# Kernel optimization log

Measured on AMD Instinct MI355X. Metric: run time of the kernel, lower is better.

## Reference

```python
import math
import jax, jax.numpy as jnp
import numpy as np

T_STEPS = 1000
NU = 1e-3
EPS = 1.0
MU = 1.0
DT = 0.01


def _ddx(f):
    # central difference d/dx on last dim, periodic
    return (jnp.roll(f, -1, -1) - jnp.roll(f, 1, -1)) * 0.5


def _ddy(f):
    return (jnp.roll(f, -1, -2) - jnp.roll(f, 1, -2)) * 0.5


def _laplacian(f):
    return (jnp.roll(f, 1, -1) + jnp.roll(f, -1, -1)
            + jnp.roll(f, 1, -2) + jnp.roll(f, -1, -2) - 4.0 * f)


def _cosine_betas(T, s=0.008):
    steps = jnp.arange(T + 1, dtype=jnp.float32)
    ac = jnp.cos((steps / T + s) / (1.0 + s) * (math.pi * 0.5)) ** 2
    ac = ac / ac[0]
    betas = 1.0 - ac[1:] / ac[:-1]
    return jnp.clip(betas, 0.0, 0.999)


def _wavenumbers(H, W):
    ky = jnp.fft.fftfreq(H, 1.0 / H).astype(jnp.float32).reshape(H, 1)
    kx = jnp.fft.rfftfreq(W, 1.0 / W).astype(jnp.float32).reshape(1, W // 2 + 1)
    return ky, kx


def _poisson_fft(rhs):
    # solve lap(phi) = rhs on periodic domain via rfft2
    H, W = rhs.shape[-2:]
    rhs_f = jnp.fft.rfft2(rhs)
    ky, kx = _wavenumbers(H, W)
    k2 = jnp.maximum(kx ** 2 + ky ** 2, 1e-10).at[0, 0].set(1.0)
    phi_f = rhs_f / (-4.0 * math.pi ** 2 * k2)
    phi_f = phi_f.at[:, 0, 0].set(0.0)
    return jnp.fft.irfft2(phi_f, s=(H, W))


def _project_div_free(Jx, Jy):
    H, W = Jx.shape[-2:]
    Jxf = jnp.fft.rfft2(Jx)
    Jyf = jnp.fft.rfft2(Jy)
    ky, kx = _wavenumbers(H, W)
    k2 = jnp.maximum(kx ** 2 + ky ** 2, 1e-10)
    div_f = kx * Jxf + ky * Jyf
    Jxf = Jxf - kx * div_f / k2
    Jyf = Jyf - ky * div_f / k2
    return jnp.fft.irfft2(Jxf, s=(H, W)), jnp.fft.irfft2(Jyf, s=(H, W))


def _l2_normalize(f):
    # F.normalize over flattened spatial dims per batch element
    norm = jnp.sqrt(jnp.sum(f * f, axis=(1, 2), keepdims=True))
    return f / jnp.maximum(norm, 1e-12)


def _forward(x0, noise, f_u, f_v, jx, jy, t):
    betas = _cosine_betas(T_STEPS)
    ac = jnp.cumprod(1.0 - betas)
    s_alpha = jnp.sqrt(ac)[t].reshape(-1, 1, 1, 1)
    s_one = jnp.sqrt(1.0 - ac)[t].reshape(-1, 1, 1, 1)
    sqrt_beta = jnp.sqrt(betas)[t].reshape(-1, 1, 1)

    # q_sample: x_t = sqrt(abar_t) x0 + sqrt(1-abar_t) eps
    xt = s_alpha * x0 + s_one * noise

    # ---- Navier-Stokes explicit Euler step (channels 0..2 = u,v,p) ----
    u, v, p = xt[:, 0], xt[:, 1], xt[:, 2]
    adv_u = u * _ddx(u) + v * _ddy(u)
    adv_v = u * _ddx(v) + v * _ddy(v)
    diff_u = NU * _laplacian(u)
    diff_v = NU * _laplacian(v)
    dp_dx, dp_dy = _ddx(p), _ddy(p)
    fu, fv = f_u, f_v
    for _ in range(3):  # fixed smoothing iterations
        fu = fu + 0.1 * _laplacian(fu)
        fv = fv + 0.1 * _laplacian(fv)
    fu = _l2_normalize(fu)
    fv = _l2_normalize(fv)
    u_new = u + DT * (-adv_u + diff_u - dp_dx) + sqrt_beta * fu
    v_new = v + DT * (-adv_v + diff_v - dp_dy) + sqrt_beta * fv
    div = _ddx(u_new) + _ddy(v_new)
    p_corr = _poisson_fft(div)
    u_new = u_new - _ddx(p_corr)
    v_new = v_new - _ddy(p_corr)
    p_new = p + p_corr

    # ---- Maxwell TM Yee half-step (channels 3..5 = Ex,Ey,Bz) ----
    Ex, Ey, Bz = xt[:, 3], xt[:, 4], xt[:, 5]
    Jx = jx * sqrt_beta
    Jy = jy * sqrt_beta
    Jx, Jy = _project_div_free(Jx, Jy)
    curl_E = _ddx(Ey) - _ddy(Ex)
    Bz_new = Bz - (DT / MU) * curl_E
    Ex_new = Ex + (DT / EPS) * _ddy(Bz_new) - (DT / EPS) * Jx
    Ey_new = Ey - (DT / EPS) * _ddx(Bz_new) - (DT / EPS) * Jy

    return jnp.stack([u_new, v_new, p_new, Ex_new, Ey_new, Bz_new], axis=1)


def setup_inputs() -> dict:
    key = jax.random.key(0)
    ks = jax.random.split(key, 7)
    B, C, H, W = 16, 6, 512, 512
    return {
        "x0": jax.random.normal(ks[0], (B, C, H, W), dtype=jnp.float32),
        "noise": jax.random.normal(ks[1], (B, C, H, W), dtype=jnp.float32),
        "f_u": jax.random.normal(ks[2], (B, H, W), dtype=jnp.float32),
        "f_v": jax.random.normal(ks[3], (B, H, W), dtype=jnp.float32),
        "jx": jax.random.normal(ks[4], (B, H, W), dtype=jnp.float32),
        "jy": jax.random.normal(ks[5], (B, H, W), dtype=jnp.float32),
        "t": jax.random.randint(ks[6], (B,), 0, 1000, dtype=jnp.int32),
    }


def reference(x0, noise, f_u, f_v, jx, jy, t):
    return _forward(x0, noise, f_u, f_v, jx, jy, t)
```

## Files before the change

kernel.cpp:

```cpp
#include <hip/hip_runtime.h>
#include <math.h>

#define PI2SQ4 39.478417604357434f
#define FSTRIDE 545
#define IDX(i) ((i) + ((i) >> 4))

__device__ __forceinline__ void wave_fence() {
  asm volatile("" ::: "memory");
  __builtin_amdgcn_wave_barrier();
}

__device__ __forceinline__ float4 ld4(const float* p) {
  return *reinterpret_cast<const float4*>(p);
}
__device__ __forceinline__ void st4(float* p, float4 v) {
  *reinterpret_cast<float4*>(p) = v;
}
__device__ __forceinline__ float fc(const float4& v, int j) {
  return j == 0 ? v.x : j == 1 ? v.y : j == 2 ? v.z : v.w;
}
__device__ __forceinline__ float fc8(const float4& a, const float4& b, int j) {
  return j < 4 ? fc(a, j) : fc(b, j - 4);
}
__device__ __forceinline__ float4 xtl4(const float* x0, const float* ns, int off,
                                       float sa, float so) {
  float4 a = ld4(x0 + off), b = ld4(ns + off);
  return make_float4(sa * a.x + so * b.x, sa * a.y + so * b.y,
                     sa * a.z + so * b.z, sa * a.w + so * b.w);
}

__device__ void wave_fft512(float2* s, const float2* tw, int lane, float isign) {
  wave_fence();
#pragma unroll
  for (int k = 0; k < 8; ++k) {
    int i = lane + (k << 6);
    int r = (int)(__brev((unsigned)i) >> 23);
    if (i < r) { float2 a = s[IDX(i)]; float2 b = s[IDX(r)]; s[IDX(i)] = b; s[IDX(r)] = a; }
  }
  wave_fence();
  for (int st = 0; st < 9; ++st) {
    int half = 1 << st;
#pragma unroll
    for (int k = 0; k < 4; ++k) {
      int bf = lane + (k << 6);
      int j = bf & (half - 1);
      int i0 = ((bf >> st) << (st + 1)) + j;
      int i1 = i0 + half;
      float2 w = tw[j << (8 - st)];
      float cw = w.x, sw = w.y * isign;
      float2 a = s[IDX(i0)], b = s[IDX(i1)];
      float tr = b.x * cw - b.y * sw;
      float ti = b.x * sw + b.y * cw;
      s[IDX(i0)] = make_float2(a.x + tr, a.y + ti);
      s[IDX(i1)] = make_float2(a.x - tr, a.y - ti);
    }
    wave_fence();
  }
}

__device__ __forceinline__ void tw_init(float2* tw, int tid) {
  if (tid < 256) {
    float sw, cw;
    __sincosf((float)tid * -0.012271846303085128f, &sw, &cw);
    tw[tid] = make_float2(cw, sw);
  }
}

__global__ __launch_bounds__(1024) void k_coef(const int* __restrict__ t,
                                               float* __restrict__ coef,
                                               float* __restrict__ norms) {
  __shared__ double l[1024];
  int i = threadIdx.x;
  if (i < 32) norms[i] = 0.f;
  const double s = 0.008;
  const double HPI = 1.5707963267948966;
  double val = 0.0;
  if (i < 1000) {
    double c0 = cos(((double)i / 1000.0 + s) / (1.0 + s) * HPI);
    double c1 = cos(((double)(i + 1) / 1000.0 + s) / (1.0 + s) * HPI);
    double beta = 1.0 - (c1 * c1) / (c0 * c0);
    beta = fmin(fmax(beta, 0.0), 0.999);
    val = log1p(-beta);
  }
  l[i] = val;
  __syncthreads();
  for (int off = 1; off < 1024; off <<= 1) {
    double add = (i >= off) ? l[i - off] : 0.0;
    __syncthreads();
    l[i] += add;
    __syncthreads();
  }
  if (i < 16) {
    int tt = t[i];
    double ac = exp(l[tt]);
    double c0 = cos(((double)tt / 1000.0 + s) / (1.0 + s) * HPI);
    double c1 = cos(((double)(tt + 1) / 1000.0 + s) / (1.0 + s) * HPI);
    double beta = 1.0 - (c1 * c1) / (c0 * c0);
    beta = fmin(fmax(beta, 0.0), 0.999);
    coef[i * 4 + 0] = (float)sqrt(ac);
    coef[i * 4 + 1] = (float)sqrt(1.0 - ac);
    coef[i * 4 + 2] = (float)sqrt(beta);
  }
}

__global__ __launch_bounds__(256) void k_smooth3(const float* __restrict__ fu,
                                                 const float* __restrict__ fv,
                                                 float* __restrict__ dst,
                                                 float* __restrict__ norms) {
  __shared__ float sA[70 * 71];
  __shared__ float sB[70 * 71];
  __shared__ float part[4];
  int slab = blockIdx.x >> 6;
  int tile = blockIdx.x & 63;
  int tx0 = (tile & 7) << 6, ty0 = (tile >> 3) << 6;
  int b = slab & 15;
  const float* src = ((slab >> 4) ? fv : fu) + ((size_t)b << 18);
  int tid = threadIdx.x;

  for (int idx = tid; idx < 70 * 70; idx += 256) {
    int cy = idx / 70, cx = idx - cy * 70;
    int gx = (tx0 + cx - 3) & 511, gy = (ty0 + cy - 3) & 511;
    sA[cy * 71 + cx] = src[(gy << 9) + gx];
  }
  __syncthreads();
  for (int idx = tid; idx < 68 * 68; idx += 256) {
    int cy = idx / 68 + 1, cx = idx % 68 + 1;
    int o = cy * 71 + cx;
    float c = sA[o];
    sB[o] = c + 0.1f * (sA[o - 1] + sA[o + 1] + sA[o - 71] + sA[o + 71] - 4.f * c);
  }
  __syncthreads();
  for (int idx = tid; idx < 66 * 66; idx += 256) {
    int cy = idx / 66 + 2, cx = idx % 66 + 2;
    int o = cy * 71 + cx;
    float c = sB[o];
    sA[o] = c + 0.1f * (sB[o - 1] + sB[o + 1] + sB[o - 71] + sB[o + 71] - 4.f * c);
  }
  __syncthreads();
  float acc = 0.f;
  float* d = dst + ((size_t)slab << 18);
  for (int idx = tid; idx < 64 * 64; idx += 256) {
    int cy = (idx >> 6) + 3, cx = (idx & 63) + 3;
    int o = cy * 71 + cx;
    float c = sA[o];
    float v = c + 0.1f * (sA[o - 1] + sA[o + 1] + sA[o - 71] + sA[o + 71] - 4.f * c);
    d[((ty0 + cy - 3) << 9) + (tx0 + cx - 3)] = v;
    acc += v * v;
  }
  for (int off = 32; off; off >>= 1) acc += __shfl_down(acc, off, 64);
  if ((tid & 63) == 0) part[tid >> 6] = acc;
  __syncthreads();
  if (tid == 0) atomicAdd(&norms[slab], part[0] + part[1] + part[2] + part[3]);
}

#define XTLS(cb, i) (sa * x0[(cb) + (i)] + so * ns[(cb) + (i)])

__global__ __launch_bounds__(256) void k_star(const float* __restrict__ x0,
    const float* __restrict__ ns, const float* __restrict__ fA,
    const float* __restrict__ coef, const float* __restrict__ norms,
    float* __restrict__ us, float* __restrict__ vs) {
  int gid = blockIdx.x * 256 + threadIdx.x;
  int x4 = (gid & 127) << 2;
  int y = (gid >> 7) & 511, b = gid >> 16;
  float sa = coef[b * 4], so = coef[b * 4 + 1], sb = coef[b * 4 + 2];
  int row = y << 9;
  int rowm = ((y + 511) & 511) << 9, rowp = ((y + 1) & 511) << 9;
  int xl = (x4 + 511) & 511, xr = (x4 + 4) & 511;
  int c0 = (b * 6) << 18, c1 = (b * 6 + 1) << 18, c2 = (b * 6 + 2) << 18;

  float4 uC = xtl4(x0, ns, c0 + row + x4, sa, so);
  float4 uU = xtl4(x0, ns, c0 + rowm + x4, sa, so);
  float4 uD = xtl4(x0, ns, c0 + rowp + x4, sa, so);
  float ulw = XTLS(c0, row + xl), urx = XTLS(c0, row + xr);
  float4 vC = xtl4(x0, ns, c1 + row + x4, sa, so);
  float4 vU = xtl4(x0, ns, c1 + rowm + x4, sa, so);
  float4 vD = xtl4(x0, ns, c1 + rowp + x4, sa, so);
  float vlw = XTLS(c1, row + xl), vrx = XTLS(c1, row + xr);
  float4 pC = xtl4(x0, ns, c2 + row + x4, sa, so);
  float4 pU = xtl4(x0, ns, c2 + rowm + x4, sa, so);
  float4 pD = xtl4(x0, ns, c2 + rowp + x4, sa, so);
  float plw = XTLS(c2, row + xl), prx = XTLS(c2, row + xr);

  float rnu = 1.f / fmaxf(sqrtf(norms[b]), 1e-12f);
  float rnv = 1.f / fmaxf(sqrtf(norms[16 + b]), 1e-12f);
  int bb = b << 18;
  float4 fu4 = ld4(fA + bb + row + x4);
  float4 fv4 = ld4(fA + ((16 + b) << 18) + row + x4);

  float ru[4], rv[4];
#pragma unroll
  for (int j = 0; j < 4; ++j) {
    float u_c = fc(uC, j), v_c = fc(vC, j);
    float u_xm = j == 0 ? ulw : fc(uC, j - 1);
    float u_xp = j == 3 ? urx : fc(uC, j + 1);
    float v_xm = j == 0 ? vlw : fc(vC, j - 1);
    float v_xp = j == 3 ? vrx : fc(vC, j + 1);
    float p_xm = j == 0 ? plw : fc(pC, j - 1);
    float p_xp = j == 3 ? prx : fc(pC, j + 1);
    float u_ym = fc(uU, j), u_yp = fc(uD, j);
    float v_ym = fc(vU, j), v_yp = fc(vD, j);
    float p_ym = fc(pU, j), p_yp = fc(pD, j);
    float adv_u = u_c * 0.5f * (u_xp - u_xm) + v_c * 0.5f * (u_yp - u_ym);
    float adv_v = u_c * 0.5f * (v_xp - v_xm) + v_c * 0.5f * (v_yp - v_ym);
    float dif_u = 0.001f * (u_xm + u_xp + u_ym + u_yp - 4.f * u_c);
    float dif_v = 0.001f * (v_xm + v_xp + v_ym + v_yp - 4.f * v_c);
    float dpx = 0.5f * (p_xp - p_xm), dpy = 0.5f * (p_yp - p_ym);
    ru[j] = u_c + 0.01f * (-adv_u + dif_u - dpx) + sb * fc(fu4, j) * rnu;
    rv[j] = v_c + 0.01f * (-adv_v + dif_v - dpy) + sb * fc(fv4, j) * rnv;
  }
  st4(us + bb + row + x4, make_float4(ru[0], ru[1], ru[2], ru[3]));
  st4(vs + bb + row + x4, make_float4(rv[0], rv[1], rv[2], rv[3]));
}

__global__ __launch_bounds__(256) void k_rowfft_div(const float* __restrict__ us,
    const float* __restrict__ vs, float2* __restrict__ spec) {
  __shared__ float2 buf[4 * FSTRIDE];
  __shared__ float2 tw[256];
  int tid = threadIdx.x;
  tw_init(tw, tid);
  int wave = tid >> 6, lane = tid & 63;
  int rid = (blockIdx.x << 2) + wave;
  int pb = rid >> 9, y = rid & 511;
  int rym = ((y + 511) & 511) << 9, ryp = ((y + 1) & 511) << 9, ry = y << 9;
  const float* ul = us + ((size_t)pb << 18);
  const float* vl = vs + ((size_t)pb << 18);
  const float* uh = us + ((size_t)(pb + 8) << 18);
  const float* vh = vs + ((size_t)(pb + 8) << 18);
  float2* s = buf + wave * FSTRIDE;
  int xx0 = lane << 3;
  int xl = (xx0 + 511) & 511, xr = (xx0 + 8) & 511;
  float4 ulA = ld4(ul + ry + xx0), ulB = ld4(ul + ry + xx0 + 4);
  float ullw = ul[ry + xl], ulrx = ul[ry + xr];
  float4 vlU0 = ld4(vl + rym + xx0), vlU1 = ld4(vl + rym + xx0 + 4);
  float4 vlD0 = ld4(vl + ryp + xx0), vlD1 = ld4(vl + ryp + xx0 + 4);
  float4 uhA = ld4(uh + ry + xx0), uhB = ld4(uh + ry + xx0 + 4);
  float uhlw = uh[ry + xl], uhrx = uh[ry + xr];
  float4 vhU0 = ld4(vh + rym + xx0), vhU1 = ld4(vh + rym + xx0 + 4);
  float4 vhD0 = ld4(vh + ryp + xx0), vhD1 = ld4(vh + ryp + xx0 + 4);
  __syncthreads();
#pragma unroll
  for (int j = 0; j < 8; ++j) {
    float uxm = j == 0 ? ullw : fc8(ulA, ulB, j - 1);
    float uxp = j == 7 ? ulrx : fc8(ulA, ulB, j + 1);
    float dlo = 0.5f * (uxp - uxm) + 0.5f * (fc8(vlD0, vlD1, j) - fc8(vlU0, vlU1, j));
    float hxm = j == 0 ? uhlw : fc8(uhA, uhB, j - 1);
    float hxp = j == 7 ? uhrx : fc8(uhA, uhB, j + 1);
    float dhi = 0.5f * (hxp - hxm) + 0.5f * (fc8(vhD0, vhD1, j) - fc8(vhU0, vhU1, j));
    s[IDX(xx0 + j)] = make_float2(dlo, dhi);
  }
  wave_fft512(s, tw, lane, 1.f);
  float2* o = spec + ((size_t)rid << 9);
#pragma unroll
  for (int j = 0; j < 4; ++j) {
    float2 a = s[IDX(xx0 + 2 * j)], b2 = s[IDX(xx0 + 2 * j + 1)];
    st4((float*)(o + xx0 + 2 * j), make_float4(a.x, a.y, b2.x, b2.y));
  }
}

__global__ __launch_bounds__(256) void k_poisson_mid(float2* __restrict__ spec) {
  __shared__ float2 buf[8 * FSTRIDE];
  __shared__ float2 tw[256];
  int tid = threadIdx.x;
  tw_init(tw, tid);
  int pb = blockIdx.x >> 6;
  int c0 = (blockIdx.x & 63) << 3;
  float2* sp = spec + ((size_t)pb << 18);
  int c = tid & 7, yb = tid >> 3;
  __syncthreads();
#pragma unroll
  for (int it = 0; it < 16; ++it) {
    int y = yb + (it << 5);
    buf[c * FSTRIDE + IDX(y)] = sp[((size_t)y << 9) + c0 + c];
  }
  __syncthreads();
  int wave = tid >> 6, lane = tid & 63;
  wave_fft512(buf + wave * FSTRIDE, tw, lane, 1.f);
  wave_fft512(buf + (wave + 4) * FSTRIDE, tw, lane, 1.f);
  __syncthreads();
  const float invN2 = 1.0f / 262144.0f;
#pragma unroll
  for (int it = 0; it < 16; ++it) {
    int y = yb + (it << 5);
    int cg = c0 + c;
    float fx = (cg < 256) ? (float)cg : (float)(cg - 512);
    float fy = (y < 256) ? (float)y : (float)(y - 512);
    float k2 = fmaxf(fx * fx + fy * fy, 1e-10f);
    float m = (cg == 0 && y == 0) ? 0.f : (-invN2 / (PI2SQ4 * k2));
    float2 v = buf[c * FSTRIDE + IDX(y)];
    buf[c * FSTRIDE + IDX(y)] = make_float2(v.x * m, v.y * m);
  }
  __syncthreads();
  wave_fft512(buf + wave * FSTRIDE, tw, lane, -1.f);
  wave_fft512(buf + (wave + 4) * FSTRIDE, tw, lane, -1.f);
  __syncthreads();
#pragma unroll
  for (int it = 0; it < 16; ++it) {
    int y = yb + (it << 5);
    sp[((size_t)y << 9) + c0 + c] = buf[c * FSTRIDE + IDX(y)];
  }
}

__global__ __launch_bounds__(256) void k_rowifft_real(const float2* __restrict__ spec,
                                                      float* __restrict__ pcorr) {
  __shared__ float2 buf[4 * FSTRIDE];
  __shared__ float2 tw[256];
  int tid = threadIdx.x;
  tw_init(tw, tid);
  int wave = tid >> 6, lane = tid & 63;
  int rid = (blockIdx.x << 2) + wave;
  int pb = rid >> 9, y = rid & 511;
  const float2* srow = spec + ((size_t)rid << 9);
  float2* s = buf + wave * FSTRIDE;
  int xx0 = lane << 3;
  const float4* s4 = reinterpret_cast<const float4*>(srow + xx0);
  float4 q0 = s4[0], q1 = s4[1], q2 = s4[2], q3 = s4[3];
  __syncthreads();
  s[IDX(xx0 + 0)] = make_float2(q0.x, q0.y);
  s[IDX(xx0 + 1)] = make_float2(q0.z, q0.w);
  s[IDX(xx0 + 2)] = make_float2(q1.x, q1.y);
  s[IDX(xx0 + 3)] = make_float2(q1.z, q1.w);
  s[IDX(xx0 + 4)] = make_float2(q2.x, q2.y);
  s[IDX(xx0 + 5)] = make_float2(q2.z, q2.w);
  s[IDX(xx0 + 6)] = make_float2(q3.x, q3.y);
  s[IDX(xx0 + 7)] = make_float2(q3.z, q3.w);
  wave_fft512(s, tw, lane, -1.f);
  float* dlo = pcorr + ((size_t)pb << 18) + ((size_t)y << 9);
  float* dhi = pcorr + ((size_t)(pb + 8) << 18) + ((size_t)y << 9);
  float2 v0 = s[IDX(xx0 + 0)], v1 = s[IDX(xx0 + 1)], v2 = s[IDX(xx0 + 2)], v3 = s[IDX(xx0 + 3)];
  float2 v4 = s[IDX(xx0 + 4)], v5 = s[IDX(xx0 + 5)], v6 = s[IDX(xx0 + 6)], v7 = s[IDX(xx0 + 7)];
  st4(dlo + xx0, make_float4(v0.x, v1.x, v2.x, v3.x));
  st4(dlo + xx0 + 4, make_float4(v4.x, v5.x, v6.x, v7.x));
  st4(dhi + xx0, make_float4(v0.y, v1.y, v2.y, v3.y));
  st4(dhi + xx0 + 4, make_float4(v4.y, v5.y, v6.y, v7.y));
}

__global__ __launch_bounds__(256) void k_fluid_out(const float* __restrict__ x0,
    const float* __restrict__ ns, const float* __restrict__ coef,
    const float* __restrict__ us, const float* __restrict__ vs,
    const float* __restrict__ pc, float* __restrict__ out) {
  int gid = blockIdx.x * 256 + threadIdx.x;
  int x4 = (gid & 127) << 2;
  int y = (gid >> 7) & 511, b = gid >> 16;
  float sa = coef[b * 4], so = coef[b * 4 + 1];
  int row = y << 9;
  int rowm = ((y + 511) & 511) << 9, rowp = ((y + 1) & 511) << 9;
  int xl = (x4 + 511) & 511, xr = (x4 + 4) & 511;
  int bb = b << 18;
  const float* pcb = pc + bb;
  float4 pCc = ld4(pcb + row + x4);
  float4 pUu = ld4(pcb + rowm + x4);
  float4 pDd = ld4(pcb + rowp + x4);
  float plw = pcb[row + xl], prx = pcb[row + xr];
  float4 us4 = ld4(us + bb + row + x4);
  float4 vs4 = ld4(vs + bb + row + x4);
  int c2 = (b * 6 + 2) << 18;
  float4 p04 = xtl4(x0, ns, c2 + row + x4, sa, so);
  float ro0[4], ro1[4], ro2[4];
#pragma unroll
  for (int j = 0; j < 4; ++j) {
    float pxm = j == 0 ? plw : fc(pCc, j - 1);
    float pxp = j == 3 ? prx : fc(pCc, j + 1);
    ro0[j] = fc(us4, j) - 0.5f * (pxp - pxm);
    ro1[j] = fc(vs4, j) - 0.5f * (fc(pDd, j) - fc(pUu, j));
    ro2[j] = fc(p04, j) + fc(pCc, j);
  }
  st4(out + ((b * 6 + 0) << 18) + row + x4, make_float4(ro0[0], ro0[1], ro0[2], ro0[3]));
  st4(out + ((b * 6 + 1) << 18) + row + x4, make_float4(ro1[0], ro1[1], ro1[2], ro1[3]));
  st4(out + c2 + row + x4, make_float4(ro2[0], ro2[1], ro2[2], ro2[3]));
}

__global__ __launch_bounds__(256) void k_rowfft_q(const float* __restrict__ jx,
    const float* __restrict__ jy, const float* __restrict__ coef,
    float2* __restrict__ spec) {
  __shared__ float2 buf[4 * FSTRIDE];
  __shared__ float2 tw[256];
  int tid = threadIdx.x;
  tw_init(tw, tid);
  int wave = tid >> 6, lane = tid & 63;
  int row = (blockIdx.x << 2) + wave;
  int b = row >> 9, y = row & 511;
  float sb = coef[b * 4 + 2];
  const float* jxr = jx + ((size_t)b << 18) + ((size_t)y << 9);
  const float* jyr = jy + ((size_t)b << 18) + ((size_t)y << 9);
  float2* s = buf + wave * FSTRIDE;
  int xx0 = lane << 3;
  float4 xA = ld4(jxr + xx0), xB = ld4(jxr + xx0 + 4);
  float4 yA = ld4(jyr + xx0), yB = ld4(jyr + xx0 + 4);
  __syncthreads();
#pragma unroll
  for (int j = 0; j < 8; ++j)
    s[IDX(xx0 + j)] = make_float2(fc8(xA, xB, j) * sb, fc8(yA, yB, j) * sb);
  wave_fft512(s, tw, lane, 1.f);
  float2* o = spec + ((size_t)row << 9);
#pragma unroll
  for (int j = 0; j < 4; ++j) {
    float2 a = s[IDX(xx0 + 2 * j)], b2 = s[IDX(xx0 + 2 * j + 1)];
    st4((float*)(o + xx0 + 2 * j), make_float4(a.x, a.y, b2.x, b2.y));
  }
}

__device__ __forceinline__ int colof(int jj, int c) {
  int col = (c < 4) ? ((jj << 2) + c) : ((512 - (jj << 2) - 3 + (c - 4)) & 511);
  if (jj == 0 && c == 7) col = 256;
  return col;
}

__device__ __forceinline__ void proj_pair(float2* buf, int jj, int cc, int yy, int mcc) {
  int my = (512 - yy) & 511;
  float2 F1 = buf[cc * FSTRIDE + IDX(yy)];
  float2 F2 = buf[mcc * FSTRIDE + IDX(my)];
  float Jxr = 0.5f * (F1.x + F2.x), Jxi = 0.5f * (F1.y - F2.y);
  float Jyr = 0.5f * (F1.y + F2.y), Jyi = 0.5f * (F2.x - F1.x);
  int colc = colof(jj, cc);
  float fx = (colc < 256) ? (float)colc : (float)(colc - 512);
  float fy = (yy < 256) ? (float)yy : (float)(yy - 512);
  float k2 = fmaxf(fx * fx + fy * fy, 1e-10f);
  float inv = 1.0f / k2;
  float Dr = fx * Jxr + fy * Jyr, Di = fx * Jxi + fy * Jyi;
  const float invN2 = 1.0f / 262144.0f;
  float Jxr2 = (Jxr - fx * Dr * inv) * invN2, Jxi2 = (Jxi - fx * Di * inv) * invN2;
  float Jyr2 = (Jyr - fy * Dr * inv) * invN2, Jyi2 = (Jyi - fy * Di * inv) * invN2;
  buf[cc * FSTRIDE + IDX(yy)]  = make_float2(Jxr2 - Jyi2, Jxi2 + Jyr2);
  buf[mcc * FSTRIDE + IDX(my)] = make_float2(Jxr2 + Jyi2, Jyr2 - Jxi2);
}

__global__ __launch_bounds__(256) void k_project_mid(float2* __restrict__ spec) {
  __shared__ float2 buf[8 * FSTRIDE];
  __shared__ float2 tw[256];
  int tid = threadIdx.x;
  tw_init(tw, tid);
  int bb = blockIdx.x >> 6;
  int jj = blockIdx.x & 63;
  float2* sp = spec + ((size_t)bb << 18);
  int c = tid & 7, yb = tid >> 3;
  int mycol = colof(jj, c);
  __syncthreads();
#pragma unroll
  for (int it = 0; it < 16; ++it) {
    int y = yb + (it << 5);
    buf[c * FSTRIDE + IDX(y)] = sp[((size_t)y << 9) + mycol];
  }
  __syncthreads();
  int wave = tid >> 6, lane = tid & 63;
  wave_fft512(buf + wave * FSTRIDE, tw, lane, 1.f);
  wave_fft512(buf + (wave + 4) * FSTRIDE, tw, lane, 1.f);
  __syncthreads();
#pragma unroll
  for (int it = 0; it < 8; ++it) {
    int tIdx = (it << 8) + tid;
    int cc = tIdx >> 9, y = tIdx & 511;
    if (jj == 0 && cc == 0) {
      if (y > 256) {
        proj_pair(buf, 0, 7, y - 256, 7);
      } else {
        proj_pair(buf, 0, 0, y, 0);
        if (y == 0 || y == 256) proj_pair(buf, 0, 7, y, 7);
      }
    } else {
      proj_pair(buf, jj, cc, y, 7 - cc);
    }
  }
  __syncthreads();
  wave_fft512(buf + wave * FSTRIDE, tw, lane, -1.f);
  wave_fft512(buf + (wave + 4) * FSTRIDE, tw, lane, -1.f);
  __syncthreads();
#pragma unroll
  for (int it = 0; it < 16; ++it) {
    int y = yb + (it << 5);
    sp[((size_t)y << 9) + mycol] = buf[c * FSTRIDE + IDX(y)];
  }
}

__global__ __launch_bounds__(256) void k_rowifft_j(const float2* __restrict__ spec,
                                                   float* __restrict__ jpx,
                                                   float* __restrict__ jpy) {
  __shared__ float2 buf[4 * FSTRIDE];
  __shared__ float2 tw[256];
  int tid = threadIdx.x;
  tw_init(tw, tid);
  int wave = tid >> 6, lane = tid & 63;
  int row = (blockIdx.x << 2) + wave;
  const float2* srow = spec + ((size_t)row << 9);
  float2* s = buf + wave * FSTRIDE;
  int xx0 = lane << 3;
  const float4* s4 = reinterpret_cast<const float4*>(srow + xx0);
  float4 q0 = s4[0], q1 = s4[1], q2 = s4[2], q3 = s4[3];
  __syncthreads();
  s[IDX(xx0 + 0)] = make_float2(q0.x, q0.y);
  s[IDX(xx0 + 1)] = make_float2(q0.z, q0.w);
  s[IDX(xx0 + 2)] = make_float2(q1.x, q1.y);
  s[IDX(xx0 + 3)] = make_float2(q1.z, q1.w);
  s[IDX(xx0 + 4)] = make_float2(q2.x, q2.y);
  s[IDX(xx0 + 5)] = make_float2(q2.z, q2.w);
  s[IDX(xx0 + 6)] = make_float2(q3.x, q3.y);
  s[IDX(xx0 + 7)] = make_float2(q3.z, q3.w);
  wave_fft512(s, tw, lane, -1.f);
  float* dx = jpx + ((size_t)row << 9);
  float* dy = jpy + ((size_t)row << 9);
  float2 v0 = s[IDX(xx0 + 0)], v1 = s[IDX(xx0 + 1)], v2 = s[IDX(xx0 + 2)], v3 = s[IDX(xx0 + 3)];
  float2 v4 = s[IDX(xx0 + 4)], v5 = s[IDX(xx0 + 5)], v6 = s[IDX(xx0 + 6)], v7 = s[IDX(xx0 + 7)];
  st4(dx + xx0, make_float4(v0.x, v1.x, v2.x, v3.x));
  st4(dx + xx0 + 4, make_float4(v4.x, v5.x, v6.x, v7.x));
  st4(dy + xx0, make_float4(v0.y, v1.y, v2.y, v3.y));
  st4(dy + xx0 + 4, make_float4(v4.y, v5.y, v6.y, v7.y));
}

__global__ __launch_bounds__(256) void k_em_bz(const float* __restrict__ x0,
    const float* __restrict__ ns, const float* __restrict__ coef,
    float* __restrict__ out) {
  int gid = blockIdx.x * 256 + threadIdx.x;
  int x4 = (gid & 127) << 2;
  int y = (gid >> 7) & 511, b = gid >> 16;
  float sa = coef[b * 4], so = coef[b * 4 + 1];
  int row = y << 9;
  int rowm = ((y + 511) & 511) << 9, rowp = ((y + 1) & 511) << 9;
  int xl = (x4 + 511) & 511, xr = (x4 + 4) & 511;
  int c3 = (b * 6 + 3) << 18, c4 = (b * 6 + 4) << 18, c5 = (b * 6 + 5) << 18;
  float4 exU = xtl4(x0, ns, c3 + rowm + x4, sa, so);
  float4 exD = xtl4(x0, ns, c3 + rowp + x4, sa, so);
  float4 eyC = xtl4(x0, ns, c4 + row + x4, sa, so);
  float eylw = XTLS(c4, row + xl), eyrx = XTLS(c4, row + xr);
  float4 bzC = xtl4(x0, ns, c5 + row + x4, sa, so);
  float r[4];
#pragma unroll
  for (int j = 0; j < 4; ++j) {
    float ey_xm = j == 0 ? eylw : fc(eyC, j - 1);
    float ey_xp = j == 3 ? eyrx : fc(eyC, j + 1);
    float curl = 0.5f * (ey_xp - ey_xm) - 0.5f * (fc(exD, j) - fc(exU, j));
    r[j] = fc(bzC, j) - 0.01f * curl;
  }
  st4(out + c5 + row + x4, make_float4(r[0], r[1], r[2], r[3]));
}

__global__ __launch_bounds__(256) void k_em_exy(const float* __restrict__ x0,
    const float* __restrict__ ns, const float* __restrict__ coef,
    const float* __restrict__ jpx, const float* __restrict__ jpy,
    float* __restrict__ out) {
  int gid = blockIdx.x * 256 + threadIdx.x;
  int x4 = (gid & 127) << 2;
  int y = (gid >> 7) & 511, b = gid >> 16;
  float sa = coef[b * 4], so = coef[b * 4 + 1];
  int row = y << 9;
  int rowm = ((y + 511) & 511) << 9, rowp = ((y + 1) & 511) << 9;
  int xl = (x4 + 511) & 511, xr = (x4 + 4) & 511;
  int c3 = (b * 6 + 3) << 18, c4 = (b * 6 + 4) << 18, c5 = (b * 6 + 5) << 18;
  const float* bzn = out + c5;
  float4 bC = ld4(bzn + row + x4);
  float4 bU = ld4(bzn + rowm + x4);
  float4 bD = ld4(bzn + rowp + x4);
  float blw = bzn[row + xl], brx = bzn[row + xr];
  float4 ex4 = xtl4(x0, ns, c3 + row + x4, sa, so);
  float4 ey4 = xtl4(x0, ns, c4 + row + x4, sa, so);
  int bb = b << 18;
  float4 jx4 = ld4(jpx + bb + row + x4);
  float4 jy4 = ld4(jpy + bb + row + x4);
  float r3[4], r4[4];
#pragma unroll
  for (int j = 0; j < 4; ++j) {
    float bxm = j == 0 ? blw : fc(bC, j - 1);
    float bxp = j == 3 ? brx : fc(bC, j + 1);
    float ddyB = 0.5f * (fc(bD, j) - fc(bU, j));
    float ddxB = 0.5f * (bxp - bxm);
    r3[j] = fc(ex4, j) + 0.01f * ddyB - 0.01f * fc(jx4, j);
    r4[j] = fc(ey4, j) - 0.01f * ddxB - 0.01f * fc(jy4, j);
  }
  st4(out + c3 + row + x4, make_float4(r3[0], r3[1], r3[2], r3[3]));
  st4(out + c4 + row + x4, make_float4(r4[0], r4[1], r4[2], r4[3]));
}

extern "C" void kernel_launch(void* const* d_in, const int* in_sizes, int n_in,
                              void* d_out, int out_size, void* d_ws, size_t ws_size,
                              hipStream_t stream) {
  const float* x0    = (const float*)d_in[0];
  const float* noise = (const float*)d_in[1];
  const float* f_u   = (const float*)d_in[2];
  const float* f_v   = (const float*)d_in[3];
  const float* jx    = (const float*)d_in[4];
  const float* jy    = (const float*)d_in[5];
  const int*   t     = (const int*)d_in[6];
  float* out = (float*)d_out;
  char* ws = (char*)d_ws;

  const size_t BHW = 1ull << 22;
  float* coef  = (float*)ws;
  float* norms = coef + 64;
  float* fA    = (float*)(ws + 1024);
  float* pcorr = fA + 2 * BHW;
  float* ustar = pcorr + BHW;
  float* vstar = ustar + BHW;
  float2* specP = (float2*)(vstar + BHW);
  float2* specJ = (float2*)ustar;
  float* jpx   = fA;
  float* jpy   = fA + BHW;

  k_coef<<<1, 1024, 0, stream>>>(t, coef, norms);

  k_smooth3<<<2048, 256, 0, stream>>>(f_u, f_v, fA, norms);

  k_star<<<4096, 256, 0, stream>>>(x0, noise, fA, coef, norms, ustar, vstar);

  k_rowfft_div<<<1024, 256, 0, stream>>>(ustar, vstar, specP);
  k_poisson_mid<<<512, 256, 0, stream>>>(specP);
  k_rowifft_real<<<1024, 256, 0, stream>>>(specP, pcorr);
  k_fluid_out<<<4096, 256, 0, stream>>>(x0, noise, coef, ustar, vstar, pcorr, out);

  k_rowfft_q<<<2048, 256, 0, stream>>>(jx, jy, coef, specJ);
  k_project_mid<<<1024, 256, 0, stream>>>(specJ);
  k_rowifft_j<<<2048, 256, 0, stream>>>(specJ, jpx, jpy);

  k_em_bz<<<4096, 256, 0, stream>>>(x0, noise, coef, out);
  k_em_exy<<<4096, 256, 0, stream>>>(x0, noise, coef, jpx, jpy, out);
}
```

Baseline: 526.5 us.

## Fuse EM Bz and Exy kernels via shared-memory halo; widen column-FFT blocks to 512 threads

Merges the two EM update kernels into one tiled kernel. Each block computes updated Bz for an 8x128 tile plus a one-cell halo into shared memory, then uses it for the Ex/Ey updates. This removes a kernel launch and the global write-then-reread of Bz, at the cost of recomputing halo rows. The Poisson and projection column-FFT kernels now launch 512 threads, so each of the 8 waves does one FFT instead of 4 waves doing two, trading serial per-wave work for more parallel waves per block.

```diff
diff --git a/kernel.cpp b/kernel.cpp
--- a/kernel.cpp
+++ b/kernel.cpp
@@ -257,7 +257,7 @@
   }
 }
 
-__global__ __launch_bounds__(256) void k_poisson_mid(float2* __restrict__ spec) {
+__global__ __launch_bounds__(512, 8) void k_poisson_mid(float2* __restrict__ spec) {
   __shared__ float2 buf[8 * FSTRIDE];
   __shared__ float2 tw[256];
   int tid = threadIdx.x;
@@ -268,19 +268,18 @@
   int c = tid & 7, yb = tid >> 3;
   __syncthreads();
 #pragma unroll
-  for (int it = 0; it < 16; ++it) {
-    int y = yb + (it << 5);
+  for (int it = 0; it < 8; ++it) {
+    int y = yb + (it << 6);
     buf[c * FSTRIDE + IDX(y)] = sp[((size_t)y << 9) + c0 + c];
   }
   __syncthreads();
   int wave = tid >> 6, lane = tid & 63;
   wave_fft512(buf + wave * FSTRIDE, tw, lane, 1.f);
-  wave_fft512(buf + (wave + 4) * FSTRIDE, tw, lane, 1.f);
   __syncthreads();
   const float invN2 = 1.0f / 262144.0f;
 #pragma unroll
-  for (int it = 0; it < 16; ++it) {
-    int y = yb + (it << 5);
+  for (int it = 0; it < 8; ++it) {
+    int y = yb + (it << 6);
     int cg = c0 + c;
     float fx = (cg < 256) ? (float)cg : (float)(cg - 512);
     float fy = (y < 256) ? (float)y : (float)(y - 512);
@@ -291,11 +290,10 @@
   }
   __syncthreads();
   wave_fft512(buf + wave * FSTRIDE, tw, lane, -1.f);
-  wave_fft512(buf + (wave + 4) * FSTRIDE, tw, lane, -1.f);
-  __syncthreads();
-#pragma unroll
-  for (int it = 0; it < 16; ++it) {
-    int y = yb + (it << 5);
+  __syncthreads();
+#pragma unroll
+  for (int it = 0; it < 8; ++it) {
+    int y = yb + (it << 6);
     sp[((size_t)y << 9) + c0 + c] = buf[c * FSTRIDE + IDX(y)];
   }
 }
@@ -424,7 +422,7 @@
   buf[mcc * FSTRIDE + IDX(my)] = make_float2(Jxr2 + Jyi2, Jyr2 - Jxi2);
 }
 
-__global__ __launch_bounds__(256) void k_project_mid(float2* __restrict__ spec) {
+__global__ __launch_bounds__(512, 8) void k_project_mid(float2* __restrict__ spec) {
   __shared__ float2 buf[8 * FSTRIDE];
   __shared__ float2 tw[256];
   int tid = threadIdx.x;
@@ -436,18 +434,17 @@
   int mycol = colof(jj, c);
   __syncthreads();
 #pragma unroll
-  for (int it = 0; it < 16; ++it) {
-    int y = yb + (it << 5);
+  for (int it = 0; it < 8; ++it) {
+    int y = yb + (it << 6);
     buf[c * FSTRIDE + IDX(y)] = sp[((size_t)y << 9) + mycol];
   }
   __syncthreads();
   int wave = tid >> 6, lane = tid & 63;
   wave_fft512(buf + wave * FSTRIDE, tw, lane, 1.f);
-  wave_fft512(buf + (wave + 4) * FSTRIDE, tw, lane, 1.f);
-  __syncthreads();
-#pragma unroll
-  for (int it = 0; it < 8; ++it) {
-    int tIdx = (it << 8) + tid;
+  __syncthreads();
+#pragma unroll
+  for (int it = 0; it < 4; ++it) {
+    int tIdx = (it << 9) + tid;
     int cc = tIdx >> 9, y = tIdx & 511;
     if (jj == 0 && cc == 0) {
       if (y > 256) {
@@ -462,11 +459,10 @@
   }
   __syncthreads();
   wave_fft512(buf + wave * FSTRIDE, tw, lane, -1.f);
-  wave_fft512(buf + (wave + 4) * FSTRIDE, tw, lane, -1.f);
-  __syncthreads();
-#pragma unroll
-  for (int it = 0; it < 16; ++it) {
-    int y = yb + (it << 5);
+  __syncthreads();
+#pragma unroll
+  for (int it = 0; it < 8; ++it) {
+    int y = yb + (it << 6);
     sp[((size_t)y << 9) + mycol] = buf[c * FSTRIDE + IDX(y)];
   }
 }
@@ -505,67 +501,77 @@
   st4(dy + xx0 + 4, make_float4(v4.y, v5.y, v6.y, v7.y));
 }
 
-__global__ __launch_bounds__(256) void k_em_bz(const float* __restrict__ x0,
-    const float* __restrict__ ns, const float* __restrict__ coef,
-    float* __restrict__ out) {
-  int gid = blockIdx.x * 256 + threadIdx.x;
-  int x4 = (gid & 127) << 2;
-  int y = (gid >> 7) & 511, b = gid >> 16;
-  float sa = coef[b * 4], so = coef[b * 4 + 1];
-  int row = y << 9;
-  int rowm = ((y + 511) & 511) << 9, rowp = ((y + 1) & 511) << 9;
-  int xl = (x4 + 511) & 511, xr = (x4 + 4) & 511;
-  int c3 = (b * 6 + 3) << 18, c4 = (b * 6 + 4) << 18, c5 = (b * 6 + 5) << 18;
-  float4 exU = xtl4(x0, ns, c3 + rowm + x4, sa, so);
-  float4 exD = xtl4(x0, ns, c3 + rowp + x4, sa, so);
-  float4 eyC = xtl4(x0, ns, c4 + row + x4, sa, so);
-  float eylw = XTLS(c4, row + xl), eyrx = XTLS(c4, row + xr);
-  float4 bzC = xtl4(x0, ns, c5 + row + x4, sa, so);
-  float r[4];
-#pragma unroll
-  for (int j = 0; j < 4; ++j) {
-    float ey_xm = j == 0 ? eylw : fc(eyC, j - 1);
-    float ey_xp = j == 3 ? eyrx : fc(eyC, j + 1);
-    float curl = 0.5f * (ey_xp - ey_xm) - 0.5f * (fc(exD, j) - fc(exU, j));
-    r[j] = fc(bzC, j) - 0.01f * curl;
-  }
-  st4(out + c5 + row + x4, make_float4(r[0], r[1], r[2], r[3]));
-}
-
-__global__ __launch_bounds__(256) void k_em_exy(const float* __restrict__ x0,
+__global__ __launch_bounds__(256) void k_em(const float* __restrict__ x0,
     const float* __restrict__ ns, const float* __restrict__ coef,
     const float* __restrict__ jpx, const float* __restrict__ jpy,
     float* __restrict__ out) {
-  int gid = blockIdx.x * 256 + threadIdx.x;
-  int x4 = (gid & 127) << 2;
-  int y = (gid >> 7) & 511, b = gid >> 16;
+  __shared__ float bzn[10][132];
+  int blk = blockIdx.x;
+  int b = blk >> 8;
+  int ty = (blk >> 2) & 63;
+  int tx = blk & 3;
+  int x0p = tx << 7;
+  int y0 = ty << 3;
+  int tid = threadIdx.x;
   float sa = coef[b * 4], so = coef[b * 4 + 1];
+  int c3 = (b * 6 + 3) << 18, c4 = (b * 6 + 4) << 18, c5 = (b * 6 + 5) << 18;
+
+  for (int idx = tid; idx < 320; idx += 256) {
+    int yy = idx >> 5, xq = idx & 31;
+    int y = (y0 - 1 + yy) & 511;
+    int xs = x0p + (xq << 2);
+    int row = y << 9;
+    int rowm = ((y + 511) & 511) << 9, rowp = ((y + 1) & 511) << 9;
+    int xl = (xs + 511) & 511, xr = (xs + 4) & 511;
+    float4 exU = xtl4(x0, ns, c3 + rowm + xs, sa, so);
+    float4 exD = xtl4(x0, ns, c3 + rowp + xs, sa, so);
+    float4 eyC = xtl4(x0, ns, c4 + row + xs, sa, so);
+    float eylw = XTLS(c4, row + xl), eyrx = XTLS(c4, row + xr);
+    float4 bzC = xtl4(x0, ns, c5 + row + xs, sa, so);
+#pragma unroll
+    for (int j = 0; j < 4; ++j) {
+      float ey_xm = j == 0 ? eylw : fc(eyC, j - 1);
+      float ey_xp = j == 3 ? eyrx : fc(eyC, j + 1);
+      float curl = 0.5f * (ey_xp - ey_xm) - 0.5f * (fc(exD, j) - fc(exU, j));
+      bzn[yy][1 + (xq << 2) + j] = fc(bzC, j) - 0.01f * curl;
+    }
+  }
+  if (tid < 20) {
+    int yy = tid % 10, side = tid / 10;
+    int x = side ? ((x0p + 128) & 511) : ((x0p + 511) & 511);
+    int y = (y0 - 1 + yy) & 511;
+    int row = y << 9;
+    int rowm = ((y + 511) & 511) << 9, rowp = ((y + 1) & 511) << 9;
+    int xl = (x + 511) & 511, xr = (x + 1) & 511;
+    float ex_ym = XTLS(c3, rowm + x), ex_yp = XTLS(c3, rowp + x);
+    float ey_xm = XTLS(c4, row + xl), ey_xp = XTLS(c4, row + xr);
+    float bz = XTLS(c5, row + x);
+    float curl = 0.5f * (ey_xp - ey_xm) - 0.5f * (ex_yp - ex_ym);
+    bzn[yy][side ? 129 : 0] = bz - 0.01f * curl;
+  }
+  __syncthreads();
+  int xq = tid & 31, yy = tid >> 5;
+  int xs = x0p + (xq << 2);
+  int y = y0 + yy;
   int row = y << 9;
-  int rowm = ((y + 511) & 511) << 9, rowp = ((y + 1) & 511) << 9;
-  int xl = (x4 + 511) & 511, xr = (x4 + 4) & 511;
-  int c3 = (b * 6 + 3) << 18, c4 = (b * 6 + 4) << 18, c5 = (b * 6 + 5) << 18;
-  const float* bzn = out + c5;
-  float4 bC = ld4(bzn + row + x4);
-  float4 bU = ld4(bzn + rowm + x4);
-  float4 bD = ld4(bzn + rowp + x4);
-  float blw = bzn[row + xl], brx = bzn[row + xr];
-  float4 ex4 = xtl4(x0, ns, c3 + row + x4, sa, so);
-  float4 ey4 = xtl4(x0, ns, c4 + row + x4, sa, so);
+  float4 ex4 = xtl4(x0, ns, c3 + row + xs, sa, so);
+  float4 ey4 = xtl4(x0, ns, c4 + row + xs, sa, so);
   int bb = b << 18;
-  float4 jx4 = ld4(jpx + bb + row + x4);
-  float4 jy4 = ld4(jpy + bb + row + x4);
-  float r3[4], r4[4];
+  float4 jx4 = ld4(jpx + bb + row + xs);
+  float4 jy4 = ld4(jpy + bb + row + xs);
+  int lx = 1 + (xq << 2);
+  float r3[4], r4[4], r5[4];
 #pragma unroll
   for (int j = 0; j < 4; ++j) {
-    float bxm = j == 0 ? blw : fc(bC, j - 1);
-    float bxp = j == 3 ? brx : fc(bC, j + 1);
-    float ddyB = 0.5f * (fc(bD, j) - fc(bU, j));
-    float ddxB = 0.5f * (bxp - bxm);
+    float ddyB = 0.5f * (bzn[2 + yy][lx + j] - bzn[yy][lx + j]);
+    float ddxB = 0.5f * (bzn[1 + yy][lx + j + 1] - bzn[1 + yy][lx + j - 1]);
     r3[j] = fc(ex4, j) + 0.01f * ddyB - 0.01f * fc(jx4, j);
     r4[j] = fc(ey4, j) - 0.01f * ddxB - 0.01f * fc(jy4, j);
-  }
-  st4(out + c3 + row + x4, make_float4(r3[0], r3[1], r3[2], r3[3]));
-  st4(out + c4 + row + x4, make_float4(r4[0], r4[1], r4[2], r4[3]));
+    r5[j] = bzn[1 + yy][lx + j];
+  }
+  st4(out + c3 + row + xs, make_float4(r3[0], r3[1], r3[2], r3[3]));
+  st4(out + c4 + row + xs, make_float4(r4[0], r4[1], r4[2], r4[3]));
+  st4(out + c5 + row + xs, make_float4(r5[0], r5[1], r5[2], r5[3]));
 }
 
 extern "C" void kernel_launch(void* const* d_in, const int* in_sizes, int n_in,
@@ -600,14 +606,13 @@
   k_star<<<4096, 256, 0, stream>>>(x0, noise, fA, coef, norms, ustar, vstar);
 
   k_rowfft_div<<<1024, 256, 0, stream>>>(ustar, vstar, specP);
-  k_poisson_mid<<<512, 256, 0, stream>>>(specP);
+  k_poisson_mid<<<512, 512, 0, stream>>>(specP);
   k_rowifft_real<<<1024, 256, 0, stream>>>(specP, pcorr);
   k_fluid_out<<<4096, 256, 0, stream>>>(x0, noise, coef, ustar, vstar, pcorr, out);
 
   k_rowfft_q<<<2048, 256, 0, stream>>>(jx, jy, coef, specJ);
-  k_project_mid<<<1024, 256, 0, stream>>>(specJ);
+  k_project_mid<<<1024, 512, 0, stream>>>(specJ);
   k_rowifft_j<<<2048, 256, 0, stream>>>(specJ, jpx, jpy);
 
-  k_em_bz<<<4096, 256, 0, stream>>>(x0, noise, coef, out);
-  k_em_exy<<<4096, 256, 0, stream>>>(x0, noise, coef, jpx, jpy, out);
-}
+  k_em<<<4096, 256, 0, stream>>>(x0, noise, coef, jpx, jpy, out);
+}
```

New measurement: 563.6 us. 7.0% more time.
